# Performance work log

Hardware: AMD Instinct MI355X
Metric: run time of the kernel (lower is better)

Reference implementation:

```python
import jax, jax.numpy as jnp
import numpy as np

N = 8192
IN_DIM = 256
OUT_DIM = 256
NEG_INF = -1000000000.0
LEAKY_SLOPE = 0.2


def setup_inputs() -> dict:
    key = jax.random.key(0)
    k_h, k_adj, k_W, k_a = jax.random.split(key, 4)
    h = jax.random.normal(k_h, (N, IN_DIM), dtype=jnp.float32)
    adj = jax.random.randint(k_adj, (N, N), 0, 2, dtype=jnp.int32)
    # learned params (nn.Linear without bias stores weight [out, in]; we keep [in, out] for x @ W)
    W = jax.random.normal(k_W, (IN_DIM, OUT_DIM), dtype=jnp.float32) / np.sqrt(IN_DIM)
    a = jax.random.normal(k_a, (OUT_DIM,), dtype=jnp.float32) / np.sqrt(OUT_DIM)
    return {"h": h, "adj": adj, "W": W, "a": a}


def reference(h, adj, W, a):
    Wh = h @ W                                   # [N, out_dim]
    f = Wh @ a                                   # [N]
    e = jax.nn.leaky_relu(f[:, None] + f[None, :], LEAKY_SLOPE)  # [N, N]
    mask = (adj > 0).astype(Wh.dtype)
    e_masked = e * mask + (1.0 - mask) * NEG_INF
    alpha = jax.nn.softmax(e_masked, axis=1)     # [N, N]
    h_prime = alpha @ Wh                         # [N, out_dim]
    return jax.nn.elu(h_prime), alpha
```

## Files before the change

kernel.cpp:

```cpp
#include <hip/hip_runtime.h>
#include <hip/hip_bf16.h>

#define NROW 8192
#define DIM 256

typedef short bf16x8 __attribute__((ext_vector_type(8)));
typedef float f32x4 __attribute__((ext_vector_type(4)));

__device__ __forceinline__ short f2bf(float x) {
    return __builtin_bit_cast(short, __float2bfloat16(x));
}

__device__ __forceinline__ void gload_lds16(const void* g, void* l) {
    __builtin_amdgcn_global_load_lds(
        (const __attribute__((address_space(1))) unsigned int*)g,
        (__attribute__((address_space(3))) unsigned int*)l, 16, 0, 0);
}

__global__ __launch_bounds__(256) void k1_whgemm(
    const float* __restrict__ h, const float* __restrict__ W,
    const float* __restrict__ a, short* __restrict__ whbT,
    float* __restrict__ f)
{
    __shared__ float hs[64][65];
    __shared__ float wsm[64][65];
    const int tid = threadIdx.x;
    const int tx = tid & 15, ty = tid >> 4;
    const int i0 = blockIdx.x * 64;
    const int n0 = blockIdx.y * 64;

    float acc[4][4];
#pragma unroll
    for (int u = 0; u < 4; ++u)
#pragma unroll
        for (int v = 0; v < 4; ++v) acc[u][v] = 0.f;

    for (int kb = 0; kb < DIM; kb += 64) {
#pragma unroll
        for (int rr = 0; rr < 4; ++rr) {
            int row = rr * 16 + ty;
            *(float4*)&hs[row][tx * 4] =
                *(const float4*)&h[(size_t)(i0 + row) * DIM + kb + tx * 4];
            *(float4*)&wsm[row][tx * 4] =
                *(const float4*)&W[(size_t)(kb + row) * DIM + n0 + tx * 4];
        }
        __syncthreads();
#pragma unroll 8
        for (int kk = 0; kk < 64; ++kk) {
            float av[4], bv[4];
#pragma unroll
            for (int u = 0; u < 4; ++u) av[u] = hs[ty * 4 + u][kk];
#pragma unroll
            for (int v = 0; v < 4; ++v) bv[v] = wsm[kk][tx * 4 + v];
#pragma unroll
            for (int u = 0; u < 4; ++u)
#pragma unroll
                for (int v = 0; v < 4; ++v) acc[u][v] += av[u] * bv[v];
        }
        __syncthreads();
    }

#pragma unroll
    for (int u = 0; u < 4; ++u)
#pragma unroll
        for (int v = 0; v < 4; ++v) hs[ty * 4 + u][tx * 4 + v] = acc[u][v];
    __syncthreads();

    {
        int r = tid >> 2, q = tid & 3;
        float s = 0.f;
#pragma unroll
        for (int c = 0; c < 16; ++c) s += hs[r][q * 16 + c] * a[n0 + q * 16 + c];
        s += __shfl_xor(s, 1);
        s += __shfl_xor(s, 2);
        if (q == 0) atomicAdd(&f[i0 + r], s);
    }

    {
        int n = tid >> 2, q = tid & 3;
        union { short s[16]; int4 i4[2]; } pk;
#pragma unroll
        for (int b = 0; b < 4; ++b)
#pragma unroll
            for (int c = 0; c < 4; ++c)
                pk.s[b * 4 + c] = f2bf(hs[q * 16 + b * 4 + c][n]);
        size_t base = ((size_t)(i0 >> 6) * 256 + n0 + n) * 64 + q * 16;
        *(int4*)&whbT[base] = pk.i4[0];
        *(int4*)&whbT[base + 8] = pk.i4[1];
    }
}

__global__ __launch_bounds__(256) void k3c_alpha(
    const int* __restrict__ adj, const float* __restrict__ f,
    float* __restrict__ alpha)
{
    const int i = blockIdx.x;
    const int tid = threadIdx.x;
    const float fi = f[i];
    const int* row = adj + (size_t)i * NROW;

    float4 tv[8];
    float sum = 0.f;
#pragma unroll
    for (int it = 0; it < 8; ++it) {
        const int j = it * 1024 + tid * 4;
        int4 av = *(const int4*)&row[j];
        float4 fv = *(const float4*)&f[j];
        float x0 = fi + fv.x, x1 = fi + fv.y, x2 = fi + fv.z, x3 = fi + fv.w;
        float4 t;
        t.x = av.x > 0 ? __expf(fmaxf(x0, 0.2f * x0)) : 0.f;
        t.y = av.y > 0 ? __expf(fmaxf(x1, 0.2f * x1)) : 0.f;
        t.z = av.z > 0 ? __expf(fmaxf(x2, 0.2f * x2)) : 0.f;
        t.w = av.w > 0 ? __expf(fmaxf(x3, 0.2f * x3)) : 0.f;
        tv[it] = t;
        sum += t.x + t.y + t.z + t.w;
    }

#pragma unroll
    for (int off = 32; off > 0; off >>= 1) sum += __shfl_xor(sum, off);
    __shared__ float red[4];
    if ((tid & 63) == 0) red[tid >> 6] = sum;
    __syncthreads();
    const float inv = 1.f / (red[0] + red[1] + red[2] + red[3]);

    float* arow = alpha + (size_t)i * NROW;
#pragma unroll
    for (int it = 0; it < 8; ++it) {
        float4 t = tv[it];
        float4 o = {t.x * inv, t.y * inv, t.z * inv, t.w * inv};
        *(float4*)&arow[it * 1024 + tid * 4] = o;
    }
}

__global__ __launch_bounds__(512, 2) void k4e_gemm(
    const float* __restrict__ alpha, const short* __restrict__ whbT,
    float* __restrict__ out0)
{
    __shared__ __align__(16) short Bs[4][16384];

    const int tid = threadIdx.x;
    const int wave = tid >> 6;
    const int lane = tid & 63;
    const int lo = lane & 15;
    const int quad = lane >> 4;
    const int q8 = quad * 8;
    const int rg = wave & 1;
    const int cg = wave >> 1;
    const int i0 = blockIdx.x * 32;

    const float* aptr = alpha + (size_t)(i0 + rg * 16 + lo) * NROW + q8;

    const int srow = lane >> 3;
    const int swz = ((lane & 7) ^ srow) * 8;

    const int bx0 = (quad ^ (lo & 7)) * 8;
    const int bx1 = ((4 + quad) ^ (lo & 7)) * 8;
    int off0[4], off1[4];
#pragma unroll
    for (int nt = 0; nt < 4; ++nt) {
        int rb = (cg * 64 + nt * 16 + lo) * 64;
        off0[nt] = rb + bx0;
        off1[nt] = rb + bx1;
    }

    f32x4 acc[4] = {};
    f32x4 aA[4], aB[4], aC[4], aD[4];

#define STAGE(buf, kt)                                                        \
    {                                                                         \
        const short* gtile = whbT + (size_t)(kt) * 16384;                     \
        _Pragma("unroll")                                                     \
        for (int s = 0; s < 4; ++s)                                           \
            gload_lds16(gtile + ((wave * 4 + s) * 8 + srow) * 64 + swz,       \
                        &Bs[buf][(wave * 4 + s) * 512]);                      \
    }

#define ALOAD(set, kt)                                                        \
    {                                                                         \
        const float* ap = aptr + (size_t)(kt) * 64;                           \
        asm volatile("global_load_dwordx4 %0, %4, off\n\t"                    \
                     "global_load_dwordx4 %1, %4, off offset:16\n\t"          \
                     "global_load_dwordx4 %2, %4, off offset:128\n\t"         \
                     "global_load_dwordx4 %3, %4, off offset:144"             \
                     : "=&v"(aA[set]), "=&v"(aB[set]),                        \
                       "=&v"(aC[set]), "=&v"(aD[set])                         \
                     : "v"(ap));                                              \
    }

#define CONSUME(c)                                                            \
    {                                                                         \
        bf16x8 af0, af1;                                                      \
        af0[0] = f2bf(aA[c][0]); af0[1] = f2bf(aA[c][1]);                     \
        af0[2] = f2bf(aA[c][2]); af0[3] = f2bf(aA[c][3]);                     \
        af0[4] = f2bf(aB[c][0]); af0[5] = f2bf(aB[c][1]);                     \
        af0[6] = f2bf(aB[c][2]); af0[7] = f2bf(aB[c][3]);                     \
        af1[0] = f2bf(aC[c][0]); af1[1] = f2bf(aC[c][1]);                     \
        af1[2] = f2bf(aC[c][2]); af1[3] = f2bf(aC[c][3]);                     \
        af1[4] = f2bf(aD[c][0]); af1[5] = f2bf(aD[c][1]);                     \
        af1[6] = f2bf(aD[c][2]); af1[7] = f2bf(aD[c][3]);                     \
        _Pragma("unroll")                                                     \
        for (int nt = 0; nt < 4; ++nt) {                                      \
            bf16x8 b0 = *(const bf16x8*)&Bs[c][off0[nt]];                     \
            acc[nt] = __builtin_amdgcn_mfma_f32_16x16x32_bf16(af0, b0,        \
                                                          acc[nt], 0, 0, 0);  \
            bf16x8 b1 = *(const bf16x8*)&Bs[c][off1[nt]];                     \
            acc[nt] = __builtin_amdgcn_mfma_f32_16x16x32_bf16(af1, b1,        \
                                                          acc[nt], 0, 0, 0);  \
        }                                                                     \
    }

#define KSTEP_FULL(kt, c)                                                     \
    {                                                                         \
        STAGE(((c) + 2) & 3, (kt) + 2);                                       \
        ALOAD(((c) + 2) & 3, (kt) + 2);                                       \
        asm volatile("s_waitcnt vmcnt(16)" ::: "memory");                     \
        __builtin_amdgcn_s_barrier();                                         \
        __builtin_amdgcn_sched_barrier(0);                                    \
        CONSUME(c)                                                            \
    }

    STAGE(0, 0); ALOAD(0, 0);
    STAGE(1, 1); ALOAD(1, 1);

#pragma unroll 1
    for (int base = 0; base < 124; base += 4) {
        KSTEP_FULL(base + 0, 0)
        KSTEP_FULL(base + 1, 1)
        KSTEP_FULL(base + 2, 2)
        KSTEP_FULL(base + 3, 3)
    }
    KSTEP_FULL(124, 0)
    KSTEP_FULL(125, 1)
    asm volatile("s_waitcnt vmcnt(8)" ::: "memory");
    __builtin_amdgcn_s_barrier();
    __builtin_amdgcn_sched_barrier(0);
    CONSUME(2)
    asm volatile("s_waitcnt vmcnt(0)" ::: "memory");
    __builtin_amdgcn_s_barrier();
    __builtin_amdgcn_sched_barrier(0);
    CONSUME(3)

#undef STAGE
#undef ALOAD
#undef CONSUME
#undef KSTEP_FULL

    const int ccb = cg * 64 + lo;
#pragma unroll
    for (int nt = 0; nt < 4; ++nt) {
#pragma unroll
        for (int c = 0; c < 4; ++c) {
            const int rr = i0 + rg * 16 + quad * 4 + c;
            float v = acc[nt][c];
            v = v > 0.f ? v : __expf(v) - 1.f;
            out0[(size_t)rr * DIM + ccb + nt * 16] = v;
        }
    }
}

extern "C" void kernel_launch(void* const* d_in, const int* in_sizes, int n_in,
                              void* d_out, int out_size, void* d_ws, size_t ws_size,
                              hipStream_t stream) {
    const float* h = (const float*)d_in[0];
    const int* adj = (const int*)d_in[1];
    const float* W = (const float*)d_in[2];
    const float* a = (const float*)d_in[3];
    float* out0 = (float*)d_out;
    float* alpha = out0 + (size_t)NROW * DIM;

    char* ws = (char*)d_ws;
    float* f = (float*)ws;
    short* whbT = (short*)(ws + 32768);

    hipMemsetAsync(f, 0, NROW * sizeof(float), stream);
    k1_whgemm<<<dim3(NROW / 64, DIM / 64), 256, 0, stream>>>(h, W, a, whbT, f);
    k3c_alpha<<<dim3(NROW), 256, 0, stream>>>(adj, f, alpha);
    k4e_gemm<<<dim3(NROW / 32), 512, 0, stream>>>(alpha, whbT, out0);
}
```

Baseline: 654.7 us.

## Deepen alpha GEMM prefetch to three stages and raise MFMA wave priority

Changes the alpha@Wh GEMM pipeline from prefetching two k-steps ahead to three. Each step now waits and hits the barrier first, then issues the next loads into the freed buffer. MFMA sections are wrapped in s_setprio to favour compute waves. The launch-bounds occupancy hint of 2 is dropped, which may raise register use and lower occupancy. The 4-buffer ring with 3 in flight means a slot is overwritten right after the barrier, so correctness depends on the barrier placement.

```diff
diff --git a/kernel.cpp b/kernel.cpp
--- a/kernel.cpp
+++ b/kernel.cpp
@@ -132,7 +132,7 @@
     }
 }
 
-__global__ __launch_bounds__(512, 2) void k4e_gemm(
+__global__ __launch_bounds__(512) void k4f_gemm(
     const float* __restrict__ alpha, const short* __restrict__ whbT,
     float* __restrict__ out0)
 {
@@ -198,6 +198,7 @@
         af1[2] = f2bf(aC[c][2]); af1[3] = f2bf(aC[c][3]);                     \
         af1[4] = f2bf(aD[c][0]); af1[5] = f2bf(aD[c][1]);                     \
         af1[6] = f2bf(aD[c][2]); af1[7] = f2bf(aD[c][3]);                     \
+        __builtin_amdgcn_s_setprio(1);                                        \
         _Pragma("unroll")                                                     \
         for (int nt = 0; nt < 4; ++nt) {                                      \
             bf16x8 b0 = *(const bf16x8*)&Bs[c][off0[nt]];                     \
@@ -207,43 +208,42 @@
             acc[nt] = __builtin_amdgcn_mfma_f32_16x16x32_bf16(af1, b1,        \
                                                           acc[nt], 0, 0, 0);  \
         }                                                                     \
-    }
-
-#define KSTEP_FULL(kt, c)                                                     \
-    {                                                                         \
-        STAGE(((c) + 2) & 3, (kt) + 2);                                       \
-        ALOAD(((c) + 2) & 3, (kt) + 2);                                       \
-        asm volatile("s_waitcnt vmcnt(16)" ::: "memory");                     \
+        __builtin_amdgcn_s_setprio(0);                                        \
+    }
+
+#define KSTEP(kt, c, DO, N)                                                   \
+    {                                                                         \
+        asm volatile("s_waitcnt vmcnt(" #N ")" ::: "memory");                 \
+        __builtin_amdgcn_sched_barrier(0);                                    \
         __builtin_amdgcn_s_barrier();                                         \
         __builtin_amdgcn_sched_barrier(0);                                    \
+        if (DO) {                                                             \
+            STAGE(((c) + 3) & 3, (kt) + 3);                                   \
+            ALOAD(((c) + 3) & 3, (kt) + 3);                                   \
+        }                                                                     \
         CONSUME(c)                                                            \
     }
 
     STAGE(0, 0); ALOAD(0, 0);
     STAGE(1, 1); ALOAD(1, 1);
+    STAGE(2, 2); ALOAD(2, 2);
 
 #pragma unroll 1
     for (int base = 0; base < 124; base += 4) {
-        KSTEP_FULL(base + 0, 0)
-        KSTEP_FULL(base + 1, 1)
-        KSTEP_FULL(base + 2, 2)
-        KSTEP_FULL(base + 3, 3)
-    }
-    KSTEP_FULL(124, 0)
-    KSTEP_FULL(125, 1)
-    asm volatile("s_waitcnt vmcnt(8)" ::: "memory");
-    __builtin_amdgcn_s_barrier();
-    __builtin_amdgcn_sched_barrier(0);
-    CONSUME(2)
-    asm volatile("s_waitcnt vmcnt(0)" ::: "memory");
-    __builtin_amdgcn_s_barrier();
-    __builtin_amdgcn_sched_barrier(0);
-    CONSUME(3)
+        KSTEP(base + 0, 0, true, 16)
+        KSTEP(base + 1, 1, true, 16)
+        KSTEP(base + 2, 2, true, 16)
+        KSTEP(base + 3, 3, true, 16)
+    }
+    KSTEP(124, 0, true, 16)
+    KSTEP(125, 1, false, 16)
+    KSTEP(126, 2, false, 8)
+    KSTEP(127, 3, false, 0)
 
 #undef STAGE
 #undef ALOAD
 #undef CONSUME
-#undef KSTEP_FULL
+#undef KSTEP
 
     const int ccb = cg * 64 + lo;
 #pragma unroll
@@ -275,5 +275,5 @@
     hipMemsetAsync(f, 0, NROW * sizeof(float), stream);
     k1_whgemm<<<dim3(NROW / 64, DIM / 64), 256, 0, stream>>>(h, W, a, whbT, f);
     k3c_alpha<<<dim3(NROW), 256, 0, stream>>>(adj, f, alpha);
-    k4e_gemm<<<dim3(NROW / 32), 512, 0, stream>>>(alpha, whbT, out0);
-}
+    k4f_gemm<<<dim3(NROW / 32), 512, 0, stream>>>(alpha, whbT, out0);
+}
```

New measurement: 661.2 us. Within noise of the previous version (+1.0%).
